# Kernel optimization log

Hardware: AMD Instinct MI355X
Metric: run time of the kernel (lower is better)

The kernel has to match this reference:

```python
import jax, jax.numpy as jnp
import numpy as np

N = 100000
E = 1600000
F_IN = 512
HID = 64
N_CLASSES = 16


def setup_inputs() -> dict:
    key = jax.random.key(0)
    k0, k1, k2, k3 = jax.random.split(key, 4)
    features = jax.random.normal(k0, (N, F_IN), dtype=jnp.float32)
    edge_idx = jax.random.randint(k1, (2, E), 0, N, dtype=jnp.int64)
    # Glorot-style init matching torch_geometric GCNConv defaults
    W1 = jax.random.normal(k2, (F_IN, HID), dtype=jnp.float32) * (1.0 / np.sqrt(F_IN))
    b1 = jnp.zeros((HID,), dtype=jnp.float32)
    W2 = jax.random.normal(k3, (HID, N_CLASSES), dtype=jnp.float32) * (1.0 / np.sqrt(HID))
    b2 = jnp.zeros((N_CLASSES,), dtype=jnp.float32)
    return {"features": features, "edge_idx": edge_idx, "W1": W1, "b1": b1, "W2": W2, "b2": b2}


def _gcn_layer(x, row, col, norm, W, b):
    # Linear transform first (out_channels < in_channels -> cheaper messages)
    h = x @ W                                   # [N, out]
    msg = h[row] * norm[:, None]                # gather + scale, [E+N, out]
    out = jax.ops.segment_sum(msg, col, num_segments=x.shape[0])  # scatter-add
    return out + b


def reference(features, edge_idx, W1, b1, W2, b2):
    n = features.shape[0]
    loop = jnp.arange(n, dtype=edge_idx.dtype)
    row = jnp.concatenate([edge_idx[0], loop])  # sources (+ self-loops)
    col = jnp.concatenate([edge_idx[1], loop])  # targets (+ self-loops)
    w = jnp.ones(row.shape[0], dtype=features.dtype)  # edge_weight=None -> ones
    # Symmetric normalization D^{-1/2} A D^{-1/2} (degree over targets)
    deg = jax.ops.segment_sum(w, col, num_segments=n)
    dinv = jnp.where(deg > 0, deg ** -0.5, 0.0)
    norm = dinv[row] * w * dinv[col]            # [E+N]

    x = jax.nn.relu(_gcn_layer(features, row, col, norm, W1, b1))
    # Dropout: eval mode (identity)
    logits = _gcn_layer(x, row, col, norm, W2, b2)
    return logits
```

## Files before the change

### kernel.cpp

```cpp
#include <hip/hip_runtime.h>

#define NN 100000
#define EE 1600000
#define FIN 512
#define HID 64
#define NC 16
#define ELLW 64
#define CPAD 16

#define KB2 391
#define BCAP2 4608
#define S1E 2048

typedef __attribute__((ext_vector_type(8))) short bf16x8;
typedef __attribute__((ext_vector_type(4))) float f32x4;

__device__ __forceinline__ unsigned short f2bf(float f) {
    union { float f; unsigned u; } v; v.f = f;
    unsigned r = v.u + 0x7FFFu + ((v.u >> 16) & 1u);
    return (unsigned short)(r >> 16);
}
__device__ __forceinline__ float asf(unsigned u) {
    union { unsigned u; float f; } v; v.u = u; return v.f;
}

__global__ void k_init(const float* __restrict__ W1, unsigned short* __restrict__ W1t,
                       unsigned* __restrict__ gcur) {
    int id = blockIdx.x * blockDim.x + threadIdx.x;
    if (id < KB2 * CPAD) gcur[id] = 0u;
    if (id < HID * FIN) {
        int c = id >> 9;
        int k = id & 511;
        W1t[id] = f2bf(W1[(size_t)k * HID + c]);
    }
}

__global__ __launch_bounds__(256) void k_bin(
    const int* __restrict__ erow, const int* __restrict__ ecol,
    unsigned* __restrict__ gcur, unsigned* __restrict__ staged) {
    __shared__ unsigned hist[512];
    __shared__ unsigned scanb[512];
    __shared__ unsigned cur[512];
    __shared__ unsigned sbase[512];
    __shared__ unsigned pk[S1E];
    __shared__ unsigned ga[S1E];
    const int t = threadIdx.x;
    const int e0 = blockIdx.x * S1E;

    hist[t] = 0; hist[t + 256] = 0;
    cur[t] = 0;  cur[t + 256] = 0;
    __syncthreads();

    unsigned pkd[8];
    int bs[8];
#pragma unroll
    for (int i = 0; i < 8; ++i) {
        int e = e0 + i * 256 + t;
        if (e < EE) {
            int c = ecol[e];
            int src = erow[e];
            int b = c >> 8;
            bs[i] = b;
            pkd[i] = (unsigned)src | ((unsigned)(c & 255) << 17);
            atomicAdd(&hist[b], 1u);
        } else {
            bs[i] = -1;
        }
    }
    __syncthreads();
    scanb[t] = hist[t];
    scanb[t + 256] = hist[t + 256];
    __syncthreads();
    for (int d = 1; d < 256; d <<= 1) {
        unsigned aA = (t >= d) ? scanb[t - d] : 0u;
        unsigned aB = (t >= d) ? scanb[256 + t - d] : 0u;
        __syncthreads();
        scanb[t] += aA;
        scanb[256 + t] += aB;
        __syncthreads();
    }
    unsigned totA = scanb[255];
    scanb[256 + t] += totA;
    __syncthreads();
    if (hist[t] > 0) sbase[t] = atomicAdd(&gcur[(size_t)t * CPAD], hist[t]);
    {
        int t2 = t + 256;
        if (t2 < KB2 && hist[t2] > 0) sbase[t2] = atomicAdd(&gcur[(size_t)t2 * CPAD], hist[t2]);
    }
    __syncthreads();
#pragma unroll
    for (int i = 0; i < 8; ++i) {
        int b = bs[i];
        if (b >= 0) {
            unsigned ls = atomicAdd(&cur[b], 1u);
            unsigned pos = scanb[b] - hist[b] + ls;
            unsigned gp = sbase[b] + ls;
            pk[pos] = pkd[i];
            ga[pos] = (gp < BCAP2) ? ((unsigned)b * BCAP2 + gp) : 0xFFFFFFFFu;
        }
    }
    __syncthreads();
    unsigned tot = scanb[511];
#pragma unroll
    for (int i = 0; i < 8; ++i) {
        unsigned idx = i * 256 + t;
        if (idx < tot && ga[idx] != 0xFFFFFFFFu) staged[ga[idx]] = pk[idx];
    }
}

__global__ __launch_bounds__(256) void k_scat2(
    const unsigned* __restrict__ gcur, const unsigned* __restrict__ staged,
    int* __restrict__ ell, unsigned* __restrict__ cnt, float* __restrict__ dinv) {
    __shared__ int tile[128 * 65];
    __shared__ unsigned lcnt[128];
    const int t = threadIdx.x;
    const int b = blockIdx.x >> 1;
    const int dl0 = (blockIdx.x & 1) << 7;
    if (t < 128) lcnt[t] = 0;
    __syncthreads();
    unsigned n = gcur[(size_t)b * CPAD];
    if (n > BCAP2) n = BCAP2;
    const unsigned base = (unsigned)b * BCAP2;
    for (unsigned idx = t; idx < n; idx += 256) {
        unsigned p = staged[base + idx];
        int dl = (int)(p >> 17) - dl0;
        if ((unsigned)dl < 128u) {
            int src = (int)(p & 0x1FFFFu);
            unsigned slot = atomicAdd(&lcnt[dl], 1u);
            if (slot < ELLW) tile[dl * 65 + slot] = src;
        }
    }
    __syncthreads();
    const int node0 = (b << 8) + dl0;
    int nrows = NN - node0;
    if (nrows > 128) nrows = 128;
    if (nrows > 0) {
        int* eout = ell + (size_t)node0 * ELLW;
        for (int i = t; i < nrows * ELLW; i += 256) {
            int row = i >> 6, col = i & 63;
            eout[i] = tile[row * 65 + col];
        }
        if (t < nrows) {
            int node = node0 + t;
            unsigned c = lcnt[t];
            cnt[node] = c;
            dinv[node] = 1.0f / sqrtf((float)(c + 1u));
        }
    }
}

#define BM 128
#define BK 64

__global__ __launch_bounds__(256) void k_gemm1(
    const float* __restrict__ A, const unsigned short* __restrict__ W1t,
    const float* __restrict__ dinv, unsigned short* __restrict__ h1s) {
    __shared__ unsigned short sA[BM * BK];
    __shared__ unsigned short sB[HID * BK];
    const int t = threadIdx.x;
    const int w = t >> 6;
    const int l = t & 63;
    const int row0 = blockIdx.x * BM;

    f32x4 acc[2][4];
#pragma unroll
    for (int fr = 0; fr < 2; ++fr)
#pragma unroll
        for (int fc = 0; fc < 4; ++fc)
            acc[fr][fc] = (f32x4){0.f, 0.f, 0.f, 0.f};

    for (int kb = 0; kb < FIN; kb += BK) {
        __syncthreads();
#pragma unroll
        for (int i = 0; i < 4; ++i) {
            int idx = i * 256 + t;
            int r = idx >> 3, g = idx & 7;
            float4 v0 = {0.f, 0.f, 0.f, 0.f}, v1 = {0.f, 0.f, 0.f, 0.f};
            if (row0 + r < NN) {
                const float* p = &A[(size_t)(row0 + r) * FIN + kb + g * 8];
                v0 = *reinterpret_cast<const float4*>(p);
                v1 = *reinterpret_cast<const float4*>(p + 4);
            }
            unsigned short tmp[8] = {f2bf(v0.x), f2bf(v0.y), f2bf(v0.z), f2bf(v0.w),
                                     f2bf(v1.x), f2bf(v1.y), f2bf(v1.z), f2bf(v1.w)};
            *reinterpret_cast<uint4*>((char*)sA + r * 128 + ((g ^ (r & 7)) << 4)) =
                *reinterpret_cast<uint4*>(tmp);
        }
#pragma unroll
        for (int i = 0; i < 2; ++i) {
            int idx = i * 256 + t;
            int c = idx >> 3, g = idx & 7;
            uint4 v = *reinterpret_cast<const uint4*>(&W1t[(size_t)c * FIN + kb + g * 8]);
            *reinterpret_cast<uint4*>((char*)sB + c * 128 + ((g ^ (c & 7)) << 4)) = v;
        }
        __syncthreads();
#pragma unroll
        for (int ks = 0; ks < 2; ++ks) {
            const int gk = ks * 4 + (l >> 4);
            bf16x8 a[2], b[4];
#pragma unroll
            for (int fr = 0; fr < 2; ++fr) {
                int r = w * 32 + fr * 16 + (l & 15);
                a[fr] = *reinterpret_cast<const bf16x8*>((char*)sA + r * 128 + ((gk ^ (r & 7)) << 4));
            }
#pragma unroll
            for (int fc = 0; fc < 4; ++fc) {
                int c = fc * 16 + (l & 15);
                b[fc] = *reinterpret_cast<const bf16x8*>((char*)sB + c * 128 + ((gk ^ (c & 7)) << 4));
            }
#pragma unroll
            for (int fr = 0; fr < 2; ++fr)
#pragma unroll
                for (int fc = 0; fc < 4; ++fc)
                    acc[fr][fc] = __builtin_amdgcn_mfma_f32_16x16x32_bf16(
                        a[fr], b[fc], acc[fr][fc], 0, 0, 0);
        }
    }
#pragma unroll
    for (int fr = 0; fr < 2; ++fr) {
#pragma unroll
        for (int r = 0; r < 4; ++r) {
            int grow = row0 + w * 32 + fr * 16 + (l >> 4) * 4 + r;
            if (grow >= NN) continue;
            float di = dinv[grow];
#pragma unroll
            for (int fc = 0; fc < 4; ++fc) {
                int col = fc * 16 + (l & 15);
                h1s[(size_t)grow * HID + col] = f2bf(acc[fr][fc][r] * di);
            }
        }
    }
}

__global__ __launch_bounds__(256) void k_agg1(
    const unsigned* __restrict__ cnt, const int* __restrict__ ell,
    const unsigned short* __restrict__ h1s, const float* __restrict__ dinv,
    const float* __restrict__ b1, unsigned short* __restrict__ x) {
    int wid = (blockIdx.x * blockDim.x + threadIdx.x) >> 6;
    if (wid >= NN) return;
    const int l = threadIdx.x & 63;
    const int g = l >> 3;
    const int q = l & 7;
    const int total = (int)cnt[wid] + 1;
    const int base = wid * ELLW;

    float a0 = 0.f, a1 = 0.f, a2 = 0.f, a3 = 0.f;
    float a4 = 0.f, a5 = 0.f, a6 = 0.f, a7 = 0.f;
    for (int s = 0; s < total; s += 8) {
        int e = s + g;
        int ee = min(e, total - 1);
        int src = (ee == 0) ? wid : ell[base + ee - 1];
        uint4 u = *reinterpret_cast<const uint4*>(&h1s[(size_t)src * HID + q * 8]);
        float m = (e < total) ? 1.f : 0.f;
        a0 = fmaf(m, asf(u.x << 16), a0);
        a1 = fmaf(m, asf(u.x & 0xFFFF0000u), a1);
        a2 = fmaf(m, asf(u.y << 16), a2);
        a3 = fmaf(m, asf(u.y & 0xFFFF0000u), a3);
        a4 = fmaf(m, asf(u.z << 16), a4);
        a5 = fmaf(m, asf(u.z & 0xFFFF0000u), a5);
        a6 = fmaf(m, asf(u.w << 16), a6);
        a7 = fmaf(m, asf(u.w & 0xFFFF0000u), a7);
    }
#pragma unroll
    for (int d = 8; d <= 32; d <<= 1) {
        a0 += __shfl_xor(a0, d); a1 += __shfl_xor(a1, d);
        a2 += __shfl_xor(a2, d); a3 += __shfl_xor(a3, d);
        a4 += __shfl_xor(a4, d); a5 += __shfl_xor(a5, d);
        a6 += __shfl_xor(a6, d); a7 += __shfl_xor(a7, d);
    }
    if (g == 0) {
        float di = dinv[wid];
        float4 bA = *reinterpret_cast<const float4*>(&b1[q * 8]);
        float4 bB = *reinterpret_cast<const float4*>(&b1[q * 8 + 4]);
        float r0 = fmaxf(fmaf(a0, di, bA.x), 0.f);
        float r1 = fmaxf(fmaf(a1, di, bA.y), 0.f);
        float r2 = fmaxf(fmaf(a2, di, bA.z), 0.f);
        float r3 = fmaxf(fmaf(a3, di, bA.w), 0.f);
        float r4 = fmaxf(fmaf(a4, di, bB.x), 0.f);
        float r5 = fmaxf(fmaf(a5, di, bB.y), 0.f);
        float r6 = fmaxf(fmaf(a6, di, bB.z), 0.f);
        float r7 = fmaxf(fmaf(a7, di, bB.w), 0.f);
        uint4 pv;
        pv.x = (unsigned)f2bf(r0) | ((unsigned)f2bf(r1) << 16);
        pv.y = (unsigned)f2bf(r2) | ((unsigned)f2bf(r3) << 16);
        pv.z = (unsigned)f2bf(r4) | ((unsigned)f2bf(r5) << 16);
        pv.w = (unsigned)f2bf(r6) | ((unsigned)f2bf(r7) << 16);
        *reinterpret_cast<uint4*>(&x[(size_t)wid * HID + q * 8]) = pv;
    }
}

__global__ __launch_bounds__(256) void k_gemm2(
    const unsigned short* __restrict__ x, const float* __restrict__ W2,
    const float* __restrict__ dinv, unsigned short* __restrict__ h2s) {
    __shared__ float sW[HID][NC];
    const int t = threadIdx.x;
#pragma unroll
    for (int i = 0; i < 4; ++i) {
        int q = t + i * 256;
        sW[q >> 4][q & 15] = W2[q];
    }
    __syncthreads();
    int i = blockIdx.x * blockDim.x + t;
    if (i >= NN) return;

    float acc[NC];
#pragma unroll
    for (int j = 0; j < NC; ++j) acc[j] = 0.f;
    const unsigned short* xr = &x[(size_t)i * HID];
#pragma unroll
    for (int k8 = 0; k8 < 8; ++k8) {
        uint4 u = *reinterpret_cast<const uint4*>(&xr[k8 * 8]);
        float f[8] = {asf(u.x << 16), asf(u.x & 0xFFFF0000u),
                      asf(u.y << 16), asf(u.y & 0xFFFF0000u),
                      asf(u.z << 16), asf(u.z & 0xFFFF0000u),
                      asf(u.w << 16), asf(u.w & 0xFFFF0000u)};
#pragma unroll
        for (int m = 0; m < 8; ++m)
#pragma unroll
            for (int j = 0; j < NC; ++j)
                acc[j] = fmaf(f[m], sW[k8 * 8 + m][j], acc[j]);
    }
    float di = dinv[i];
    unsigned short hv[NC];
#pragma unroll
    for (int j = 0; j < NC; ++j) hv[j] = f2bf(acc[j] * di);
    *reinterpret_cast<uint4*>(&h2s[(size_t)i * NC])     = *reinterpret_cast<uint4*>(hv);
    *reinterpret_cast<uint4*>(&h2s[(size_t)i * NC + 8]) = *reinterpret_cast<uint4*>(hv + 8);
}

__global__ __launch_bounds__(256) void k_agg2(
    const unsigned* __restrict__ cnt, const int* __restrict__ ell,
    const unsigned short* __restrict__ h2s, const float* __restrict__ dinv,
    const float* __restrict__ b2, float* __restrict__ out) {
    int wid = (blockIdx.x * blockDim.x + threadIdx.x) >> 6;
    if (wid >= NN) return;
    const int l = threadIdx.x & 63;
    const int g = l >> 1;
    const int q = l & 1;
    const int total = (int)cnt[wid] + 1;
    const int base = wid * ELLW;

    float a0 = 0.f, a1 = 0.f, a2 = 0.f, a3 = 0.f;
    float a4 = 0.f, a5 = 0.f, a6 = 0.f, a7 = 0.f;
    for (int s = 0; s < total; s += 32) {
        int e = s + g;
        int ee = min(e, total - 1);
        int src = (ee == 0) ? wid : ell[base + ee - 1];
        uint4 u = *reinterpret_cast<const uint4*>(&h2s[(size_t)src * NC + q * 8]);
        float m = (e < total) ? 1.f : 0.f;
        a0 = fmaf(m, asf(u.x << 16), a0);
        a1 = fmaf(m, asf(u.x & 0xFFFF0000u), a1);
        a2 = fmaf(m, asf(u.y << 16), a2);
        a3 = fmaf(m, asf(u.y & 0xFFFF0000u), a3);
        a4 = fmaf(m, asf(u.z << 16), a4);
        a5 = fmaf(m, asf(u.z & 0xFFFF0000u), a5);
        a6 = fmaf(m, asf(u.w << 16), a6);
        a7 = fmaf(m, asf(u.w & 0xFFFF0000u), a7);
    }
#pragma unroll
    for (int d = 2; d <= 32; d <<= 1) {
        a0 += __shfl_xor(a0, d); a1 += __shfl_xor(a1, d);
        a2 += __shfl_xor(a2, d); a3 += __shfl_xor(a3, d);
        a4 += __shfl_xor(a4, d); a5 += __shfl_xor(a5, d);
        a6 += __shfl_xor(a6, d); a7 += __shfl_xor(a7, d);
    }
    if (g == 0) {
        float di = dinv[wid];
        float4 bA = *reinterpret_cast<const float4*>(&b2[q * 8]);
        float4 bB = *reinterpret_cast<const float4*>(&b2[q * 8 + 4]);
        float4 w0, w1;
        w0.x = fmaf(a0, di, bA.x); w0.y = fmaf(a1, di, bA.y);
        w0.z = fmaf(a2, di, bA.z); w0.w = fmaf(a3, di, bA.w);
        w1.x = fmaf(a4, di, bB.x); w1.y = fmaf(a5, di, bB.y);
        w1.z = fmaf(a6, di, bB.z); w1.w = fmaf(a7, di, bB.w);
        *reinterpret_cast<float4*>(&out[(size_t)wid * NC + q * 8])     = w0;
        *reinterpret_cast<float4*>(&out[(size_t)wid * NC + q * 8 + 4]) = w1;
    }
}

extern "C" void kernel_launch(void* const* d_in, const int* in_sizes, int n_in,
                              void* d_out, int out_size, void* d_ws, size_t ws_size,
                              hipStream_t stream) {
    const float* features = (const float*)d_in[0];
    const int*   edges    = (const int*)d_in[1];
    const float* W1       = (const float*)d_in[2];
    const float* b1       = (const float*)d_in[3];
    const float* W2       = (const float*)d_in[4];
    const float* b2       = (const float*)d_in[5];
    float* out = (float*)d_out;

    const int* erow = edges;
    const int* ecol = edges + EE;

    char* ws = (char*)d_ws;
    size_t o = 0;
    auto alloc = [&](size_t bytes) { size_t p = o; o = (o + bytes + 255) & ~255ULL; return p; };
    unsigned*       gcur  = (unsigned*)      (ws + alloc((size_t)KB2 * CPAD * 4));
    unsigned*       cnt   = (unsigned*)      (ws + alloc((size_t)NN * 4));
    float*          dinv  = (float*)         (ws + alloc((size_t)NN * 4));
    unsigned*       staged= (unsigned*)      (ws + alloc((size_t)KB2 * BCAP2 * 4));
    unsigned short* W1t   = (unsigned short*)(ws + alloc((size_t)HID * FIN * 2));
    int*            ell   = (int*)           (ws + alloc((size_t)(KB2 << 8) * ELLW * 4));
    unsigned short* h1s   = (unsigned short*)(ws + alloc((size_t)NN * HID * 2));
    unsigned short* x     = (unsigned short*)(ws + alloc((size_t)NN * HID * 2));
    unsigned short* h2s   = (unsigned short*)(ws + alloc((size_t)NN * NC * 2));

    k_init <<<128, 256, 0, stream>>>(W1, W1t, gcur);
    k_bin  <<<(EE + S1E - 1) / S1E, 256, 0, stream>>>(erow, ecol, gcur, staged);
    k_scat2<<<KB2 * 2, 256, 0, stream>>>(gcur, staged, ell, cnt, dinv);
    k_gemm1<<<(NN + BM - 1) / BM, 256, 0, stream>>>(features, W1t, dinv, h1s);
    k_agg1 <<<NN / 4, 256, 0, stream>>>(cnt, ell, h1s, dinv, b1, x);
    k_gemm2<<<(NN + 255) / 256, 256, 0, stream>>>(x, W2, dinv, h2s);
    k_agg2 <<<NN / 4, 256, 0, stream>>>(cnt, ell, h2s, dinv, b2, out);
}
```

Baseline: 193.8 us.

## Enlarge edge binning chunks and write staged bins with per-wave coalesced stores

The binning kernel now handles 8192 edges per block instead of 2048, so far fewer blocks issue global atomics on the per-bin cursors and each bin's chunk is larger. Edges are read twice (once for the histogram, once for placement) rather than held in registers, and the per-slot global address array is removed. The final write walks each bin with one wave so consecutive lanes store to consecutive staged slots. The cost is a second pass over the edge arrays and fewer blocks to spread across the GPU.

Measured after the change: 218.4 us. 1.13x slower.

```diff
diff --git a/kernel.cpp b/kernel.cpp
--- a/kernel.cpp
+++ b/kernel.cpp
@@ -10,7 +10,8 @@
 
 #define KB2 391
 #define BCAP2 4608
-#define S1E 2048
+#define S1E 8192
+#define NBIN ((EE + S1E - 1) / S1E)
 
 typedef __attribute__((ext_vector_type(8))) short bf16x8;
 typedef __attribute__((ext_vector_type(4))) float f32x4;
@@ -43,7 +44,6 @@
     __shared__ unsigned cur[512];
     __shared__ unsigned sbase[512];
     __shared__ unsigned pk[S1E];
-    __shared__ unsigned ga[S1E];
     const int t = threadIdx.x;
     const int e0 = blockIdx.x * S1E;
 
@@ -51,21 +51,10 @@
     cur[t] = 0;  cur[t + 256] = 0;
     __syncthreads();
 
-    unsigned pkd[8];
-    int bs[8];
-#pragma unroll
-    for (int i = 0; i < 8; ++i) {
-        int e = e0 + i * 256 + t;
-        if (e < EE) {
-            int c = ecol[e];
-            int src = erow[e];
-            int b = c >> 8;
-            bs[i] = b;
-            pkd[i] = (unsigned)src | ((unsigned)(c & 255) << 17);
-            atomicAdd(&hist[b], 1u);
-        } else {
-            bs[i] = -1;
-        }
+#pragma unroll 8
+    for (int k = 0; k < 32; ++k) {
+        int e = e0 + k * 256 + t;
+        if (e < EE) atomicAdd(&hist[ecol[e] >> 8], 1u);
     }
     __syncthreads();
     scanb[t] = hist[t];
@@ -88,23 +77,27 @@
         if (t2 < KB2 && hist[t2] > 0) sbase[t2] = atomicAdd(&gcur[(size_t)t2 * CPAD], hist[t2]);
     }
     __syncthreads();
-#pragma unroll
-    for (int i = 0; i < 8; ++i) {
-        int b = bs[i];
-        if (b >= 0) {
+#pragma unroll 4
+    for (int k = 0; k < 32; ++k) {
+        int e = e0 + k * 256 + t;
+        if (e < EE) {
+            int c = ecol[e];
+            int b = c >> 8;
             unsigned ls = atomicAdd(&cur[b], 1u);
-            unsigned pos = scanb[b] - hist[b] + ls;
-            unsigned gp = sbase[b] + ls;
-            pk[pos] = pkd[i];
-            ga[pos] = (gp < BCAP2) ? ((unsigned)b * BCAP2 + gp) : 0xFFFFFFFFu;
-        }
-    }
-    __syncthreads();
-    unsigned tot = scanb[511];
-#pragma unroll
-    for (int i = 0; i < 8; ++i) {
-        unsigned idx = i * 256 + t;
-        if (idx < tot && ga[idx] != 0xFFFFFFFFu) staged[ga[idx]] = pk[idx];
+            pk[(scanb[b] - hist[b]) + ls] = (unsigned)erow[e] | ((unsigned)(c & 255) << 17);
+        }
+    }
+    __syncthreads();
+    const int wv = t >> 6, ln = t & 63;
+    for (int b = wv; b < KB2; b += 4) {
+        unsigned h = hist[b];
+        if (h == 0) continue;
+        unsigned ex = scanb[b] - h;
+        unsigned gb = sbase[b];
+        for (unsigned j = ln; j < h; j += 64) {
+            unsigned gp = gb + j;
+            if (gp < BCAP2) staged[(size_t)b * BCAP2 + gp] = pk[ex + j];
+        }
     }
 }
 
@@ -406,7 +399,7 @@
     unsigned short* h2s   = (unsigned short*)(ws + alloc((size_t)NN * NC * 2));
 
     k_init <<<128, 256, 0, stream>>>(W1, W1t, gcur);
-    k_bin  <<<(EE + S1E - 1) / S1E, 256, 0, stream>>>(erow, ecol, gcur, staged);
+    k_bin  <<<NBIN, 256, 0, stream>>>(erow, ecol, gcur, staged);
     k_scat2<<<KB2 * 2, 256, 0, stream>>>(gcur, staged, ell, cnt, dinv);
     k_gemm1<<<(NN + BM - 1) / BM, 256, 0, stream>>>(features, W1t, dinv, h1s);
     k_agg1 <<<NN / 4, 256, 0, stream>>>(cnt, ell, h1s, dinv, b1, x);
```
